# Kernel tuning notes

Hardware: AMD Instinct MI355X
Metric: run time of the kernel (lower is better)

## Reference

```python
import jax, jax.numpy as jnp
import numpy as np

N = 200_000
E = 6_400_000
EPS = 1e-12


def l2_normalize(x):
    # F.normalize(x, p=2, dim=1): x / max(||x||_2, eps)
    n = jnp.linalg.norm(x, axis=1, keepdims=True)
    return x / jnp.maximum(n, EPS)


def gcn_conv(x, W, b, src, dst, n):
    """PyG GCNConv: add self-loops, symmetric normalization D^-1/2 A D^-1/2,
    linear transform (no bias) on nodes, scatter-add to targets, then + bias."""
    loop = jnp.arange(n)
    s = jnp.concatenate([src, loop])  # sources (messages gathered here)
    d = jnp.concatenate([dst, loop])  # targets (aggregation here)
    deg = jax.ops.segment_sum(jnp.ones(s.shape[0], dtype=x.dtype), d, num_segments=n)
    dinv = jnp.where(deg > 0, jax.lax.rsqrt(deg), 0.0)
    norm = dinv[s] * dinv[d]  # [E+N]
    h = x @ W  # [N, out]
    out = jax.ops.segment_sum(norm[:, None] * h[s], d, num_segments=n)
    return out + b


def setup_inputs() -> dict:
    key = jax.random.key(0)
    ks = jax.random.split(key, 10)
    x = jax.random.normal(ks[0], (N, 3), dtype=jnp.float32)
    edge_index = jax.random.randint(ks[1], (2, E), 0, N, dtype=jnp.int64)

    def glorot(k, shape):
        lim = float(np.sqrt(6.0 / (shape[0] + shape[1])))
        return jax.random.uniform(k, shape, jnp.float32, -lim, lim)

    return {
        "x": x,
        "edge_index": edge_index,
        "W1": glorot(ks[2], (3, 6)),   "b1": jnp.zeros((6,), jnp.float32),
        "W2": glorot(ks[3], (6, 12)),  "b2": jnp.zeros((12,), jnp.float32),
        "W3": glorot(ks[4], (12, 24)), "b3": jnp.zeros((24,), jnp.float32),
        "Wc": glorot(ks[5], (24, 13)), "bc": jnp.zeros((13,), jnp.float32),
    }


def reference(x, edge_index, W1, b1, W2, b2, W3, b3, Wc, bc):
    src, dst = edge_index[0], edge_index[1]
    n = x.shape[0]
    h = jnp.tanh(gcn_conv(x, W1, b1, src, dst, n))
    h = jnp.tanh(l2_normalize(gcn_conv(h, W2, b2, src, dst, n)))
    h = l2_normalize(gcn_conv(h, W3, b3, src, dst, n))
    h = h @ Wc + bc
    return l2_normalize(h)
```

## Files before the change

kernel.cpp:

```cpp
#include <hip/hip_runtime.h>
#include <math.h>


static constexpr int NN = 200000;
static constexpr int NE = 6400000;
static constexpr int BK = 256;

static constexpr int SUBW  = 512;
static constexpr int NBA   = (NN + SUBW - 1) / SUBW;
static constexpr int CAP   = 24;
static constexpr int FLUSH = 16;
static constexpr int CAPB  = 18400;
static constexpr int BKP   = 512;
static constexpr int EPT   = 4;
static constexpr int CHUNK = BKP * EPT;
static constexpr int GPART = 1024;
static constexpr int SRCSH = 13;
static constexpr int NSB   = (NN + (1 << SRCSH) - 1) >> SRCSH;

static constexpr int S     = 4;
static constexpr int LOGS  = 2;

__global__ void __launch_bounds__(BKP) k_part(const int* __restrict__ srcI,
                                              const int* __restrict__ dstI,
                                              unsigned* __restrict__ stg,
                                              int* __restrict__ gtail, int e) {
  __shared__ unsigned bin[CAP][NBA];
  __shared__ int bcnt[NBA];
  for (int t = threadIdx.x; t < NBA; t += BKP) bcnt[t] = 0;
  __syncthreads();
  int nchunks = (e + CHUNK - 1) / CHUNK;
  for (int c = blockIdx.x; c < nchunks; c += gridDim.x) {
    int base_i = c * CHUNK;
    int dv[EPT], sv[EPT];
#pragma unroll
    for (int u = 0; u < EPT; ++u) {
      int i = base_i + u * BKP + (int)threadIdx.x;
      dv[u] = (i < e) ? __builtin_nontemporal_load(dstI + i) : -1;
      sv[u] = (i < e) ? __builtin_nontemporal_load(srcI + i) : 0;
    }
#pragma unroll
    for (int u = 0; u < EPT; ++u) {
      if (dv[u] >= 0) {
        int b = dv[u] >> 9;
        unsigned rec = ((unsigned)(dv[u] & (SUBW - 1)) << 18) | (unsigned)sv[u];
        int p = atomicAdd(&bcnt[b], 1);
        if (p < CAP) {
          bin[p][b] = rec;
        } else {
          int base = atomicAdd(&gtail[b], 1);
          stg[(size_t)b * CAPB + base] = rec;
        }
      }
    }
    __syncthreads();
    int b2 = threadIdx.x;
    if (b2 < NBA) {
      int c2 = bcnt[b2];
      if (c2 > CAP) c2 = CAP;
      if (c2 >= FLUSH) {
        int nfl = c2 & ~(FLUSH - 1);
        int base = atomicAdd(&gtail[b2], nfl);
        size_t o = (size_t)b2 * CAPB + base;
        for (int k = 0; k < nfl; k += 4) {
          uint4 v;
          v.x = bin[k][b2]; v.y = bin[k + 1][b2]; v.z = bin[k + 2][b2]; v.w = bin[k + 3][b2];
          *(uint4*)(stg + o + k) = v;
        }
        int r = c2 - nfl;
        for (int k = 0; k < r; ++k) bin[k][b2] = bin[nfl + k][b2];
        bcnt[b2] = r;
      }
    }
    __syncthreads();
  }
  int b2 = threadIdx.x;
  if (b2 < NBA) {
    int c2 = bcnt[b2];
    if (c2 > CAP) c2 = CAP;
    if (c2 > 0) {
      int base = atomicAdd(&gtail[b2], c2);
      size_t o = (size_t)b2 * CAPB + base;
      for (int k = 0; k < c2; ++k) stg[o + k] = bin[k][b2];
    }
  }
}

__global__ void k_scan_sub(const int* __restrict__ gtail, int* __restrict__ sbase) {
  __shared__ int s0[512], s1[512];
  int t = threadIdx.x;
  int v = (t < NBA) ? gtail[t] : 0;
  s0[t] = v;
  __syncthreads();
  int* a = s0; int* b = s1;
  for (int off = 1; off < 512; off <<= 1) {
    int x = a[t] + ((t >= off) ? a[t - off] : 0);
    b[t] = x;
    __syncthreads();
    int* tmp = a; a = b; b = tmp;
  }
  if (t < NBA) sbase[t] = a[t] - v;
}

__global__ void __launch_bounds__(BK) k_build(const unsigned* __restrict__ stg,
                                              const int* __restrict__ gtail,
                                              const int* __restrict__ sbase,
                                              int* __restrict__ rowptr,
                                              int* __restrict__ adj,
                                              int* __restrict__ b8,
                                              int* __restrict__ b13,
                                              int* __restrict__ b17) {
  __shared__ unsigned hist2[SUBW * NSB];
  __shared__ int htot[SUBW];
  __shared__ int s0[SUBW], s1[SUBW];
  int b = blockIdx.x;
  int m = gtail[b]; if (m > CAPB) m = CAPB;
  size_t off = (size_t)b * CAPB;
  int base = sbase[b];
  if (b == NBA - 1 && threadIdx.x == 0) rowptr[NN] = base + m;
  for (int t = threadIdx.x; t < SUBW * NSB; t += BK) hist2[t] = 0;
  __syncthreads();
  for (int k = threadIdx.x; k < m; k += BK) {
    unsigned rec = stg[off + k];
    int dl = rec >> 18;
    int sb = (int)((rec & 0x3FFFFu) >> SRCSH);
    atomicAdd(&hist2[dl * NSB + sb], 1u);
  }
  __syncthreads();
  for (int dl = threadIdx.x; dl < SUBW; dl += BK) {
    unsigned run = 0;
    for (int sb = 0; sb < NSB; ++sb) {
      unsigned c = hist2[dl * NSB + sb];
      hist2[dl * NSB + sb] = run;
      run += c;
    }
    htot[dl] = (int)run;
    s0[dl] = (int)run;
  }
  __syncthreads();
  int* a = s0; int* bb = s1;
  for (int o2 = 1; o2 < SUBW; o2 <<= 1) {
    for (int t = threadIdx.x; t < SUBW; t += BK) bb[t] = a[t] + ((t >= o2) ? a[t - o2] : 0);
    __syncthreads();
    int* tmp = a; a = bb; bb = tmp;
  }
  for (int t = threadIdx.x; t < SUBW; t += BK) {
    int node = b * SUBW + t;
    int ex = a[t] - htot[t];
    if (node < NN) {
      rowptr[node] = base + ex;
      b8[node]  = base + ex + (int)hist2[t * NSB + 8];
      b13[node] = base + ex + (int)hist2[t * NSB + 13];
      b17[node] = base + ex + (int)hist2[t * NSB + 17];
    }
    bb[t] = ex;
  }
  __syncthreads();
  for (int k = threadIdx.x; k < m; k += BK) {
    unsigned rec = stg[off + k];
    int dl = rec >> 18;
    unsigned src = rec & 0x3FFFFu;
    int sb = (int)(src >> SRCSH);
    int p = bb[dl] + (int)atomicAdd(&hist2[dl * NSB + sb], 1u);
    adj[base + p] = (int)src;
  }
}

__global__ void k_zero(int* __restrict__ p, int n) {
  int i = blockIdx.x * blockDim.x + threadIdx.x;
  if (i < n) p[i] = 0;
}

__global__ void k_dinv(const int* __restrict__ rowptr, float* __restrict__ dinv, int n) {
  int i = blockIdx.x * blockDim.x + threadIdx.x;
  if (i < n) dinv[i] = rsqrtf(1.0f + (float)(rowptr[i + 1] - rowptr[i]));
}

__global__ void k_prep(const float* __restrict__ x, const float* __restrict__ dinv,
                       float* __restrict__ p1, int n) {
  int i = blockIdx.x * blockDim.x + threadIdx.x;
  if (i >= n) return;
  float di = dinv[i];
  float3 v;
  v.x = di * x[3 * (size_t)i];
  v.y = di * x[3 * (size_t)i + 1];
  v.z = di * x[3 * (size_t)i + 2];
  *(float3*)(p1 + 3 * (size_t)i) = v;
}

template <int RW> struct RowT;
template <> struct RowT<3> {
  using T = float3;
  static __device__ inline T ld(const float* __restrict__ p) { return *(const float3*)p; }
  static __device__ inline void add(float* __restrict__ a, const T& v) {
    a[0] += v.x; a[1] += v.y; a[2] += v.z;
  }
  static __device__ inline void st(float* __restrict__ p, const float* __restrict__ a) {
    *(float3*)p = make_float3(a[0], a[1], a[2]);
  }
};
template <> struct RowT<6> {
  struct T { float2 a, b, c; };
  static __device__ inline T ld(const float* __restrict__ p) {
    T t; t.a = *(const float2*)p; t.b = *(const float2*)(p + 2); t.c = *(const float2*)(p + 4);
    return t;
  }
  static __device__ inline void add(float* __restrict__ a, const T& v) {
    a[0] += v.a.x; a[1] += v.a.y; a[2] += v.b.x; a[3] += v.b.y; a[4] += v.c.x; a[5] += v.c.y;
  }
  static __device__ inline void st(float* __restrict__ p, const float* __restrict__ a) {
    *(float2*)(p)     = make_float2(a[0], a[1]);
    *(float2*)(p + 2) = make_float2(a[2], a[3]);
    *(float2*)(p + 4) = make_float2(a[4], a[5]);
  }
};
template <> struct RowT<12> {
  struct T { float4 a, b, c; };
  static __device__ inline T ld(const float* __restrict__ p) {
    T t; t.a = *(const float4*)p; t.b = *(const float4*)(p + 4); t.c = *(const float4*)(p + 8);
    return t;
  }
  static __device__ inline void add(float* __restrict__ a, const T& v) {
    a[0] += v.a.x; a[1] += v.a.y; a[2] += v.a.z; a[3] += v.a.w;
    a[4] += v.b.x; a[5] += v.b.y; a[6] += v.b.z; a[7] += v.b.w;
    a[8] += v.c.x; a[9] += v.c.y; a[10] += v.c.z; a[11] += v.c.w;
  }
  static __device__ inline void st(float* __restrict__ p, const float* __restrict__ a) {
    *(float4*)(p)     = make_float4(a[0], a[1], a[2], a[3]);
    *(float4*)(p + 4) = make_float4(a[4], a[5], a[6], a[7]);
    *(float4*)(p + 8) = make_float4(a[8], a[9], a[10], a[11]);
  }
};

template <int RW, int UN>
__device__ inline void gather_p(const int* __restrict__ adj, int st, int en,
                                const float* __restrict__ pin, float* __restrict__ acc,
                                int slot) {
  using RT = RowT<RW>;
  using T = typename RT::T;
  int k = st + slot;
  if (k + (UN - 1) * S < en) {
    int a[UN];
#pragma unroll
    for (int u = 0; u < UN; ++u) a[u] = adj[k + u * S];
    for (;;) {
      int kn = k + UN * S;
      bool more = (kn + (UN - 1) * S < en);
      int b[UN];
#pragma unroll
      for (int u = 0; u < UN; ++u) b[u] = 0;
      if (more) {
#pragma unroll
        for (int u = 0; u < UN; ++u) b[u] = adj[kn + u * S];
      }
      T v[UN];
#pragma unroll
      for (int u = 0; u < UN; ++u) v[u] = RT::ld(pin + (size_t)a[u] * RW);
#pragma unroll
      for (int u = 0; u < UN; ++u) RT::add(acc, v[u]);
      k = kn;
      if (!more) break;
#pragma unroll
      for (int u = 0; u < UN; ++u) a[u] = b[u];
    }
  }
  for (; k < en; k += S) {
    T v = RT::ld(pin + (size_t)adj[k] * RW);
    RT::add(acc, v);
  }
}

template <int FIN>
__device__ inline void group_reduce(float* __restrict__ acc) {
#pragma unroll
  for (int j = 0; j < FIN; ++j) {
    acc[j] += __shfl_xor(acc[j], 1);
    acc[j] += __shfl_xor(acc[j], 2);
  }
}

template <int RW, int FOUT, int MODE>
__global__ void __launch_bounds__(BK, 8) k_gather_fused(
    const int* __restrict__ adj, const int* __restrict__ rowptr,
    const float* __restrict__ pin, const float* __restrict__ W,
    const float* __restrict__ bias, const float* __restrict__ dinv,
    float* __restrict__ pout, int n) {
  __shared__ float sW[RW * FOUT];
  __shared__ float sb[FOUT];
  for (int t = threadIdx.x; t < RW * FOUT; t += BK) sW[t] = W[t];
  if (threadIdx.x < FOUT) sb[threadIdx.x] = bias[threadIdx.x];
  __syncthreads();
  int g = blockIdx.x * blockDim.x + threadIdx.x;
  int i = g >> LOGS;
  int slot = g & (S - 1);
  if (i >= n) return;
  float acc[RW] = {};
  if (slot == 0) {
    typename RowT<RW>::T v = RowT<RW>::ld(pin + (size_t)i * RW);
    RowT<RW>::add(acc, v);
  }
  gather_p<RW, 4>(adj, rowptr[i], rowptr[i + 1], pin, acc, slot);
  group_reduce<RW>(acc);
  float di = dinv[i];
  float h[FOUT];
  float ss = 0.f;
#pragma unroll
  for (int j = 0; j < FOUT; ++j) {
    float s = 0.f;
#pragma unroll
    for (int kk = 0; kk < RW; ++kk) s = fmaf(acc[kk], sW[kk * FOUT + j], s);
    float t = fmaf(di, s, sb[j]);
    h[j] = t;
    ss += t * t;
  }
  float o[FOUT];
  if (MODE == 0) {
#pragma unroll
    for (int j = 0; j < FOUT; ++j) o[j] = di * tanhf(h[j]);
  } else {
    float inv = 1.f / fmaxf(sqrtf(ss), 1e-12f);
#pragma unroll
    for (int j = 0; j < FOUT; ++j) o[j] = di * tanhf(h[j] * inv);
  }
  if (slot == 0) {
    float* po = pout + (size_t)i * FOUT;
    if (MODE == 0) {
      *(float2*)(po)     = make_float2(o[0], o[1]);
      *(float2*)(po + 2) = make_float2(o[2], o[3]);
      *(float2*)(po + 4) = make_float2(o[4], o[5]);
    } else {
      *(float4*)(po)     = make_float4(o[0], o[1], o[2], o[3]);
      *(float4*)(po + 4) = make_float4(o[4], o[5], o[6], o[7]);
      *(float4*)(po + 8) = make_float4(o[8], o[9], o[10], o[11]);
    }
  }
}

template <int RW, bool FIRST>
__global__ void __launch_bounds__(BK, 8) k_gphase(
    const int* __restrict__ adj, const int* __restrict__ stA,
    const int* __restrict__ enB, const float* __restrict__ pin,
    float* __restrict__ accb, int n) {
  int g = blockIdx.x * blockDim.x + threadIdx.x;
  int i = g >> LOGS;
  int slot = g & (S - 1);
  if (i >= n) return;
  float acc[RW] = {};
  if (slot == 0) {
    if (FIRST) {
      typename RowT<RW>::T v = RowT<RW>::ld(pin + (size_t)i * RW);
      RowT<RW>::add(acc, v);
    } else {
      typename RowT<RW>::T v = RowT<RW>::ld(accb + (size_t)i * RW);
      RowT<RW>::add(acc, v);
    }
  }
  gather_p<RW, 2>(adj, stA[i], enB[i], pin, acc, slot);
  group_reduce<RW>(acc);
  if (slot == 0) RowT<RW>::st(accb + (size_t)i * RW, acc);
}

template <int RW, int FOUT, int MODE>
__global__ void __launch_bounds__(BK, 6) k_gphase_last(
    const int* __restrict__ adj, const int* __restrict__ stA,
    const int* __restrict__ rowptr, const float* __restrict__ pin,
    const float* __restrict__ W, const float* __restrict__ bias,
    const float* __restrict__ Wc, const float* __restrict__ bc,
    const float* __restrict__ dinv, const float* __restrict__ accb,
    float* __restrict__ out, int n) {
  constexpr int FC = 13;
  __shared__ float sW[RW * FOUT];
  __shared__ float sb[FOUT];
  __shared__ float sWc[MODE == 2 ? FOUT * FC : 1];
  __shared__ float sbc[MODE == 2 ? FC : 1];
  for (int t = threadIdx.x; t < RW * FOUT; t += BK) sW[t] = W[t];
  if (threadIdx.x < FOUT) sb[threadIdx.x] = bias[threadIdx.x];
  if (MODE == 2) {
    for (int t = threadIdx.x; t < FOUT * FC; t += BK) sWc[t] = Wc[t];
    if (threadIdx.x < FC) sbc[threadIdx.x] = bc[threadIdx.x];
  }
  __syncthreads();
  int g = blockIdx.x * blockDim.x + threadIdx.x;
  int i = g >> LOGS;
  int slot = g & (S - 1);
  if (i >= n) return;
  float acc[RW] = {};
  if (slot == 0) {
    typename RowT<RW>::T v = RowT<RW>::ld(accb + (size_t)i * RW);
    RowT<RW>::add(acc, v);
  }
  gather_p<RW, 2>(adj, stA[i], rowptr[i + 1], pin, acc, slot);
  group_reduce<RW>(acc);
  float di = dinv[i];
  float h[FOUT];
  float ss = 0.f;
#pragma unroll
  for (int j = 0; j < FOUT; ++j) {
    float s = 0.f;
#pragma unroll
    for (int kk = 0; kk < RW; ++kk) s = fmaf(acc[kk], sW[kk * FOUT + j], s);
    float t = fmaf(di, s, sb[j]);
    h[j] = t;
    ss += t * t;
  }
  float inv = 1.f / fmaxf(sqrtf(ss), 1e-12f);
  if (MODE == 1) {
    float o[FOUT];
#pragma unroll
    for (int j = 0; j < FOUT; ++j) o[j] = di * tanhf(h[j] * inv);
    if (slot == 0) {
      float* po = out + (size_t)i * FOUT;
      *(float4*)(po)     = make_float4(o[0], o[1], o[2], o[3]);
      *(float4*)(po + 4) = make_float4(o[4], o[5], o[6], o[7]);
      *(float4*)(po + 8) = make_float4(o[8], o[9], o[10], o[11]);
    }
  } else {
    float v[FC];
    float ss2 = 0.f;
#pragma unroll
    for (int j = 0; j < FC; ++j) {
      float s = sbc[j];
#pragma unroll
      for (int kk = 0; kk < FOUT; ++kk) s = fmaf(h[kk] * inv, sWc[kk * FC + j], s);
      v[j] = s;
      ss2 += s * s;
    }
    float inv2 = 1.f / fmaxf(sqrtf(ss2), 1e-12f);
    if (slot == 0) {
#pragma unroll
      for (int j = 0; j < FC; ++j) out[(size_t)i * FC + j] = v[j] * inv2;
    }
  }
}

extern "C" void kernel_launch(void* const* d_in, const int* in_sizes, int n_in,
                              void* d_out, int out_size, void* d_ws, size_t ws_size,
                              hipStream_t stream) {
  const float* x  = (const float*)d_in[0];
  const int*   ei = (const int*)d_in[1];
  const float* W1 = (const float*)d_in[2];
  const float* b1 = (const float*)d_in[3];
  const float* W2 = (const float*)d_in[4];
  const float* b2 = (const float*)d_in[5];
  const float* W3 = (const float*)d_in[6];
  const float* b3 = (const float*)d_in[7];
  const float* Wc = (const float*)d_in[8];
  const float* bc = (const float*)d_in[9];
  float* out = (float*)d_out;

  const int n = NN;
  const int e = NE;
  const int* srcI = ei;
  const int* dstI = ei + e;

  float* ws = (float*)d_ws;
  float* dinv  = ws;
  int* rowptr  = (int*)(ws + n);
  int* gtail   = rowptr + n + 8;
  int* sbase   = gtail + 512;
  int* adj     = sbase + 512;
  int* b8      = adj + e;
  int* b13     = b8 + n;
  int* b17     = b13 + n;
  size_t roff = (size_t)n + (n + 8) + 512 + 512 + e + 3 * (size_t)n;
  roff = (roff + 15) & ~(size_t)15;
  float* R     = ws + roff;
  unsigned* stg = (unsigned*)R;
  float* p1   = R;
  float* p2   = R + (size_t)3 * n;
  float* p3   = R + (size_t)9 * n;
  float* accb = R + (size_t)21 * n;

  const int gn  = (n + BK - 1) / BK;
  const int gnS = (n * S + BK - 1) / BK;

  k_zero<<<2, BK, 0, stream>>>(gtail, 512);
  k_part<<<GPART, BKP, 0, stream>>>(srcI, dstI, stg, gtail, e);
  k_scan_sub<<<1, 512, 0, stream>>>(gtail, sbase);
  k_build<<<NBA, BK, 0, stream>>>(stg, gtail, sbase, rowptr, adj, b8, b13, b17);
  k_dinv<<<gn, BK, 0, stream>>>(rowptr, dinv, n);

  k_prep<<<gn, BK, 0, stream>>>(x, dinv, p1, n);

  k_gather_fused<3, 6, 0><<<gnS, BK, 0, stream>>>(adj, rowptr, p1, W1, b1, dinv, p2, n);

  k_gphase<6, true><<<gnS, BK, 0, stream>>>(adj, rowptr, b13, p2, accb, n);
  k_gphase_last<6, 12, 1><<<gnS, BK, 0, stream>>>(adj, b13, rowptr, p2, W2, b2,
                                                  Wc, bc, dinv, accb, p3, n);

  k_gphase<12, true><<<gnS, BK, 0, stream>>>(adj, rowptr, b8, p3, accb, n);
  k_gphase<12, false><<<gnS, BK, 0, stream>>>(adj, b8, b17, p3, accb, n);
  k_gphase_last<12, 24, 2><<<gnS, BK, 0, stream>>>(adj, b17, rowptr, p3, W3, b3,
                                                   Wc, bc, dinv, accb, out, n);
}
```

Measured before the change: 453.7 us.

## Fuse scan into build, dynamic chunking in partition, transpose bins, wider gather unroll

The partition kernel now takes chunks from a global atomic work counter instead of a fixed grid-stride loop, and its shared bins are transposed to [bucket][slot] so a flush can copy a uint4 straight out of contiguous shared memory. The separate scan kernel is removed: each build block sums the preceding bucket counts itself with a block reduction. The dinv kernel is merged into the prep kernel, and the gather unroll factor in the phase kernels rises from 2 to 4. Together these cut launch count and aim to improve load balance and memory-level parallelism. The trade-offs are redundant per-block prefix work, possible shared-memory bank conflicts from the new bin layout, and higher register pressure from the larger unroll.

```diff
diff --git a/kernel.cpp b/kernel.cpp
--- a/kernel.cpp
+++ b/kernel.cpp
@@ -24,13 +24,19 @@
 __global__ void __launch_bounds__(BKP) k_part(const int* __restrict__ srcI,
                                               const int* __restrict__ dstI,
                                               unsigned* __restrict__ stg,
-                                              int* __restrict__ gtail, int e) {
-  __shared__ unsigned bin[CAP][NBA];
+                                              int* __restrict__ gtail,
+                                              int* __restrict__ work, int e) {
+  __shared__ unsigned bin[NBA][CAP];
   __shared__ int bcnt[NBA];
+  __shared__ int curc;
   for (int t = threadIdx.x; t < NBA; t += BKP) bcnt[t] = 0;
   __syncthreads();
   int nchunks = (e + CHUNK - 1) / CHUNK;
-  for (int c = blockIdx.x; c < nchunks; c += gridDim.x) {
+  for (;;) {
+    if (threadIdx.x == 0) curc = atomicAdd(work, 1);
+    __syncthreads();
+    int c = curc;
+    if (c >= nchunks) break;
     int base_i = c * CHUNK;
     int dv[EPT], sv[EPT];
 #pragma unroll
@@ -46,7 +52,7 @@
         unsigned rec = ((unsigned)(dv[u] & (SUBW - 1)) << 18) | (unsigned)sv[u];
         int p = atomicAdd(&bcnt[b], 1);
         if (p < CAP) {
-          bin[p][b] = rec;
+          bin[b][p] = rec;
         } else {
           int base = atomicAdd(&gtail[b], 1);
           stg[(size_t)b * CAPB + base] = rec;
@@ -62,13 +68,10 @@
         int nfl = c2 & ~(FLUSH - 1);
         int base = atomicAdd(&gtail[b2], nfl);
         size_t o = (size_t)b2 * CAPB + base;
-        for (int k = 0; k < nfl; k += 4) {
-          uint4 v;
-          v.x = bin[k][b2]; v.y = bin[k + 1][b2]; v.z = bin[k + 2][b2]; v.w = bin[k + 3][b2];
-          *(uint4*)(stg + o + k) = v;
-        }
+        for (int k = 0; k < nfl; k += 4)
+          *(uint4*)(stg + o + k) = *(const uint4*)&bin[b2][k];
         int r = c2 - nfl;
-        for (int k = 0; k < r; ++k) bin[k][b2] = bin[nfl + k][b2];
+        for (int k = 0; k < r; ++k) bin[b2][k] = bin[b2][nfl + k];
         bcnt[b2] = r;
       }
     }
@@ -81,30 +84,13 @@
     if (c2 > 0) {
       int base = atomicAdd(&gtail[b2], c2);
       size_t o = (size_t)b2 * CAPB + base;
-      for (int k = 0; k < c2; ++k) stg[o + k] = bin[k][b2];
-    }
-  }
-}
-
-__global__ void k_scan_sub(const int* __restrict__ gtail, int* __restrict__ sbase) {
-  __shared__ int s0[512], s1[512];
-  int t = threadIdx.x;
-  int v = (t < NBA) ? gtail[t] : 0;
-  s0[t] = v;
-  __syncthreads();
-  int* a = s0; int* b = s1;
-  for (int off = 1; off < 512; off <<= 1) {
-    int x = a[t] + ((t >= off) ? a[t - off] : 0);
-    b[t] = x;
-    __syncthreads();
-    int* tmp = a; a = b; b = tmp;
-  }
-  if (t < NBA) sbase[t] = a[t] - v;
+      for (int k = 0; k < c2; ++k) stg[o + k] = bin[b2][k];
+    }
+  }
 }
 
 __global__ void __launch_bounds__(BK) k_build(const unsigned* __restrict__ stg,
                                               const int* __restrict__ gtail,
-                                              const int* __restrict__ sbase,
                                               int* __restrict__ rowptr,
                                               int* __restrict__ adj,
                                               int* __restrict__ b8,
@@ -113,10 +99,21 @@
   __shared__ unsigned hist2[SUBW * NSB];
   __shared__ int htot[SUBW];
   __shared__ int s0[SUBW], s1[SUBW];
+  __shared__ int red[BK];
   int b = blockIdx.x;
+  {
+    int ssum = 0;
+    for (int t = threadIdx.x; t < b; t += BK) ssum += gtail[t];
+    red[threadIdx.x] = ssum;
+    __syncthreads();
+    for (int o = BK / 2; o > 0; o >>= 1) {
+      if (threadIdx.x < o) red[threadIdx.x] += red[threadIdx.x + o];
+      __syncthreads();
+    }
+  }
+  int base = red[0];
   int m = gtail[b]; if (m > CAPB) m = CAPB;
   size_t off = (size_t)b * CAPB;
-  int base = sbase[b];
   if (b == NBA - 1 && threadIdx.x == 0) rowptr[NN] = base + m;
   for (int t = threadIdx.x; t < SUBW * NSB; t += BK) hist2[t] = 0;
   __syncthreads();
@@ -171,16 +168,12 @@
   if (i < n) p[i] = 0;
 }
 
-__global__ void k_dinv(const int* __restrict__ rowptr, float* __restrict__ dinv, int n) {
-  int i = blockIdx.x * blockDim.x + threadIdx.x;
-  if (i < n) dinv[i] = rsqrtf(1.0f + (float)(rowptr[i + 1] - rowptr[i]));
-}
-
-__global__ void k_prep(const float* __restrict__ x, const float* __restrict__ dinv,
-                       float* __restrict__ p1, int n) {
+__global__ void k_prep(const float* __restrict__ x, const int* __restrict__ rowptr,
+                       float* __restrict__ dinv, float* __restrict__ p1, int n) {
   int i = blockIdx.x * blockDim.x + threadIdx.x;
   if (i >= n) return;
-  float di = dinv[i];
+  float di = rsqrtf(1.0f + (float)(rowptr[i + 1] - rowptr[i]));
+  dinv[i] = di;
   float3 v;
   v.x = di * x[3 * (size_t)i];
   v.y = di * x[3 * (size_t)i + 1];
@@ -355,7 +348,7 @@
       RowT<RW>::add(acc, v);
     }
   }
-  gather_p<RW, 2>(adj, stA[i], enB[i], pin, acc, slot);
+  gather_p<RW, 4>(adj, stA[i], enB[i], pin, acc, slot);
   group_reduce<RW>(acc);
   if (slot == 0) RowT<RW>::st(accb + (size_t)i * RW, acc);
 }
@@ -389,7 +382,7 @@
     typename RowT<RW>::T v = RowT<RW>::ld(accb + (size_t)i * RW);
     RowT<RW>::add(acc, v);
   }
-  gather_p<RW, 2>(adj, stA[i], rowptr[i + 1], pin, acc, slot);
+  gather_p<RW, 4>(adj, stA[i], rowptr[i + 1], pin, acc, slot);
   group_reduce<RW>(acc);
   float di = dinv[i];
   float h[FOUT];
@@ -457,12 +450,12 @@
   float* dinv  = ws;
   int* rowptr  = (int*)(ws + n);
   int* gtail   = rowptr + n + 8;
-  int* sbase   = gtail + 512;
-  int* adj     = sbase + 512;
+  int* work    = gtail + 512;
+  int* adj     = work + 16;
   int* b8      = adj + e;
   int* b13     = b8 + n;
   int* b17     = b13 + n;
-  size_t roff = (size_t)n + (n + 8) + 512 + 512 + e + 3 * (size_t)n;
+  size_t roff = (size_t)n + (n + 8) + 512 + 16 + e + 3 * (size_t)n;
   roff = (roff + 15) & ~(size_t)15;
   float* R     = ws + roff;
   unsigned* stg = (unsigned*)R;
@@ -474,13 +467,11 @@
   const int gn  = (n + BK - 1) / BK;
   const int gnS = (n * S + BK - 1) / BK;
 
-  k_zero<<<2, BK, 0, stream>>>(gtail, 512);
-  k_part<<<GPART, BKP, 0, stream>>>(srcI, dstI, stg, gtail, e);
-  k_scan_sub<<<1, 512, 0, stream>>>(gtail, sbase);
-  k_build<<<NBA, BK, 0, stream>>>(stg, gtail, sbase, rowptr, adj, b8, b13, b17);
-  k_dinv<<<gn, BK, 0, stream>>>(rowptr, dinv, n);
-
-  k_prep<<<gn, BK, 0, stream>>>(x, dinv, p1, n);
+  k_zero<<<3, BK, 0, stream>>>(gtail, 528);
+  k_part<<<GPART, BKP, 0, stream>>>(srcI, dstI, stg, gtail, work, e);
+  k_build<<<NBA, BK, 0, stream>>>(stg, gtail, rowptr, adj, b8, b13, b17);
+
+  k_prep<<<gn, BK, 0, stream>>>(x, rowptr, dinv, p1, n);
 
   k_gather_fused<3, 6, 0><<<gnS, BK, 0, stream>>>(adj, rowptr, p1, W1, b1, dinv, p2, n);
 
```

New measurement: 463.3 us. +2.1%, slower.
